# Performance work log

Hardware: AMD Instinct MI355X
Metric: run time of the kernel (lower is better)

The kernel has to match this reference:

```python
import jax, jax.numpy as jnp
import numpy as np


def setup_inputs() -> dict:
    key = jax.random.key(0)
    ks = jax.random.split(key, 6)
    b, c, h, w = 4, 64, 64, 64
    hid = 32
    x = jax.random.normal(ks[0], (b, c, h, w), dtype=jnp.float32)
    sc_in = 1.0 / np.sqrt(c)
    sc_hid = 1.0 / np.sqrt(hid)
    wq = jax.random.normal(ks[1], (hid, c), dtype=jnp.float32) * sc_in
    wk = jax.random.normal(ks[2], (hid, c), dtype=jnp.float32) * sc_in
    wv = jax.random.normal(ks[3], (hid, c), dtype=jnp.float32) * sc_in
    wp = jax.random.normal(ks[4], (c, hid), dtype=jnp.float32) * sc_hid
    bq = jnp.zeros((hid,), jnp.float32)
    bk = jnp.zeros((hid,), jnp.float32)
    bv = jnp.zeros((hid,), jnp.float32)
    bp = jnp.zeros((c,), jnp.float32)
    return {"x": x, "wq": wq, "bq": bq, "wk": wk, "bk": bk,
            "wv": wv, "bv": bv, "wp": wp, "bp": bp}


def reference(x, wq, bq, wk, bk, wv, bv, wp, bp):
    b, c, h, w = x.shape
    hid = wq.shape[0]
    # flatten spatial: [b, c, n]
    xf = x.reshape(b, c, h * w)
    # 1x1 convs == channel linear: q,k,v are [b, hid, n]
    q = jnp.einsum('oc,bcn->bon', wq, xf) + bq[None, :, None]
    k = jnp.einsum('oc,bcn->bon', wk, xf) + bk[None, :, None]
    v = jnp.einsum('oc,bcn->bon', wv, xf) + bv[None, :, None]
    # attention scores: query [b,n,hid] @ key [b,hid,m] -> [b,n,m] (NO scaling, as in source)
    scores = jnp.einsum('bhn,bhm->bnm', q, k)
    attn = jax.nn.softmax(scores, axis=-1)
    # z = attn @ value^T -> [b, n, hid] -> [b, hid, n]
    z = jnp.einsum('bnm,bhm->bhn', attn, v)
    # output projection (1x1 conv) + residual
    out = xf + jnp.einsum('ch,bhn->bcn', wp, z) + bp[None, :, None]
    return out.reshape(b, c, h, w)
```

## Files before the change

kernel.cpp:

```cpp
#include <hip/hip_runtime.h>
#include <hip/hip_bf16.h>
#include <math.h>

#define BB 4
#define CC 64
#define HID 32
#define NN 4096
#define LOG2E 1.44269504088896f

typedef short sh4 __attribute__((ext_vector_type(4)));
typedef short sh8 __attribute__((ext_vector_type(8)));
typedef float f4v __attribute__((ext_vector_type(4)));

#define MFMA32(A,B,C) __builtin_amdgcn_mfma_f32_16x16x32_bf16(A,B,C,0,0,0)

__device__ __forceinline__ short f2b(float f) {
    __hip_bfloat16 h = __float2bfloat16(f);
    union { __hip_bfloat16 hb; short s; } u; u.hb = h; return u.s;
}

__global__ __launch_bounds__(512) void qkv_kernel(
    const float* __restrict__ x,
    const float* __restrict__ wq, const float* __restrict__ bq,
    const float* __restrict__ wk, const float* __restrict__ bk,
    const float* __restrict__ wv, const float* __restrict__ bv,
    short* __restrict__ Qw, short* __restrict__ Kw, short* __restrict__ Vtp)
{
    __shared__ float xs[64][80];
    __shared__ float ws[96][80];
    __shared__ float bs[96];

    const int t  = threadIdx.x;
    const int b  = blockIdx.x >> 6;
    const int n0 = (blockIdx.x & 63) << 6;

    #pragma unroll
    for (int kl = 0; kl < 2; ++kl) {
        int idx = t + 512*kl;
        int c = idx >> 4, j4 = (idx & 15) << 2;
        *(f4v*)&xs[c][j4] = *(const f4v*)(x + ((size_t)(b*CC + c))*NN + n0 + j4);
    }
    #pragma unroll
    for (int kl = 0; kl < 3; ++kl) {
        int idx = t + 512*kl;
        int r = idx >> 4, c4 = (idx & 15) << 2;
        const float* src = (r < 32) ? (wq + r*CC + c4)
                         : (r < 64) ? (wk + (r-32)*CC + c4)
                                    : (wv + (r-64)*CC + c4);
        *(f4v*)&ws[r][c4] = *(const f4v*)src;
    }
    if (t < 96) bs[t] = (t < 32) ? bq[t] : (t < 64) ? bk[t-32] : bv[t-64];
    __syncthreads();

    const int hg = t & 31;
    const int j0 = (t >> 5) << 2;

    float aq[4], ak[4], av[4];
    #pragma unroll
    for (int jj = 0; jj < 4; ++jj) { aq[jj]=bs[hg]; ak[jj]=bs[32+hg]; av[jj]=bs[64+hg]; }

    #pragma unroll
    for (int cs = 0; cs < 16; ++cs) {
        f4v wqv = *(f4v*)&ws[hg][cs*4];
        f4v wkv = *(f4v*)&ws[32+hg][cs*4];
        f4v wvv = *(f4v*)&ws[64+hg][cs*4];
        #pragma unroll
        for (int cc = 0; cc < 4; ++cc) {
            f4v xv = *(f4v*)&xs[cs*4+cc][j0];
            #pragma unroll
            for (int jj = 0; jj < 4; ++jj) {
                aq[jj] += wqv[cc]*xv[jj];
                ak[jj] += wkv[cc]*xv[jj];
                av[jj] += wvv[cc]*xv[jj];
            }
        }
    }

    const size_t nbase = (size_t)b*NN + n0 + j0;
    #pragma unroll
    for (int jj = 0; jj < 4; ++jj) {
        Qw[(nbase + jj)*HID + hg] = f2b(aq[jj] * LOG2E);
        Kw[(nbase + jj)*HID + hg] = f2b(ak[jj]);
    }
    const int w0 = j0 & 31, g = (w0 >> 2) & 3, hi = w0 >> 4;
    sh4 vv;
    #pragma unroll
    for (int jj = 0; jj < 4; ++jj) vv[jj] = f2b(av[jj]);
    *(sh4*)(Vtp + ((size_t)b*HID + hg)*NN + n0 + (j0 & ~31) + 8*g + 4*hi) = vv;
}

__global__ __launch_bounds__(512, 2) void attn_kernel(
    const short* __restrict__ Qw, const short* __restrict__ Kw,
    const short* __restrict__ Vtp, const float* __restrict__ x,
    const float* __restrict__ wp, const float* __restrict__ bp,
    float* __restrict__ out)
{
    __shared__ float zr[4][32][65];
    __shared__ float lr4[4][64];

    const int t    = threadIdx.x;
    const int b    = blockIdx.x >> 6;
    const int q0   = (blockIdx.x & 63) << 6;
    const int lane = t & 63;
    const int kq   = t >> 6;
    const int g    = lane >> 4;
    const int qi   = lane & 15;

    const short* qbase = Qw + ((size_t)b*NN + q0 + qi)*HID + 8*g;
    sh8 qf[4];
    #pragma unroll
    for (int S = 0; S < 4; ++S) qf[S] = *(const sh8*)(qbase + S*16*HID);

    const short* kp = Kw  + ((size_t)b*NN  + kq*512 + qi)*HID + 8*g;
    const short* vp = Vtp + ((size_t)b*HID + qi)*NN + kq*512 + 8*g;

    const f4v zf = {0.f,0.f,0.f,0.f};
    f4v z0[4], z1[4], lz[4];
    #pragma unroll
    for (int S = 0; S < 4; ++S) { z0[S] = zf; z1[S] = zf; lz[S] = zf; }

    sh8 ones;
    #pragma unroll
    for (int j = 0; j < 8; ++j) ones[j] = (short)0x3F80;

    sh8 a0 = *(const sh8*)kp;
    sh8 a1 = *(const sh8*)(kp + 512);
    sh8 v0 = *(const sh8*)vp;
    sh8 v1 = *(const sh8*)(vp + 16*NN);

    for (int it = 0; it < 16; ++it) {
        const int nx = (it < 15) ? it + 1 : it;
        const short* kn = kp + nx*1024;
        const short* vn = vp + nx*32;
        sh8 na0 = *(const sh8*)kn;
        sh8 na1 = *(const sh8*)(kn + 512);
        sh8 nv0 = *(const sh8*)vn;
        sh8 nv1 = *(const sh8*)(vn + 16*NN);

        f4v s0[4], s1[4];
        #pragma unroll
        for (int S = 0; S < 4; ++S) {
            s0[S] = MFMA32(a0, qf[S], zf);
            s1[S] = MFMA32(a1, qf[S], zf);
        }

        sh8 p[4];
        #pragma unroll
        for (int S = 0; S < 4; ++S) {
            float e[8];
            #pragma unroll
            for (int r = 0; r < 4; ++r) {
                e[r]   = __builtin_amdgcn_exp2f(s0[S][r]);
                e[4+r] = __builtin_amdgcn_exp2f(s1[S][r]);
            }
            #pragma unroll
            for (int j = 0; j < 8; ++j) p[S][j] = f2b(e[j]);
        }

        #pragma unroll
        for (int S = 0; S < 4; ++S) {
            z0[S] = MFMA32(v0, p[S], z0[S]);
            z1[S] = MFMA32(v1, p[S], z1[S]);
            lz[S] = MFMA32(ones, p[S], lz[S]);
        }

        a0 = na0; a1 = na1; v0 = nv0; v1 = nv1;
    }

    if (kq >= 4) {
        #pragma unroll
        for (int S = 0; S < 4; ++S) {
            #pragma unroll
            for (int r = 0; r < 4; ++r) {
                zr[kq-4][4*g+r][S*16+qi]    = z0[S][r];
                zr[kq-4][16+4*g+r][S*16+qi] = z1[S][r];
            }
            if (g == 0) lr4[kq-4][S*16+qi] = lz[S][0];
        }
    }
    __syncthreads();
    if (kq < 4) {
        #pragma unroll
        for (int S = 0; S < 4; ++S) {
            #pragma unroll
            for (int r = 0; r < 4; ++r) {
                zr[kq][4*g+r][S*16+qi]    += z0[S][r];
                zr[kq][16+4*g+r][S*16+qi] += z1[S][r];
            }
            if (g == 0) lr4[kq][S*16+qi] += lz[S][0];
        }
    }
    __syncthreads();

    if (kq < 4) {
        const int q = kq*16 + qi;
        float lm = (lr4[0][q] + lr4[1][q]) + (lr4[2][q] + lr4[3][q]);
        f4v zm0 = zf, zm1 = zf;
        #pragma unroll
        for (int j = 0; j < 4; ++j) {
            #pragma unroll
            for (int r = 0; r < 4; ++r) {
                zm0[r] += zr[j][4*g+r][q];
                zm1[r] += zr[j][16+4*g+r][q];
            }
        }
        const float inv = 1.f / lm;
        sh8 pz;
        #pragma unroll
        for (int r = 0; r < 4; ++r) {
            pz[r]   = f2b(zm0[r]*inv);
            pz[4+r] = f2b(zm1[r]*inv);
        }
        const int qcol = q0 + q;
        #pragma unroll
        for (int ct = 0; ct < 4; ++ct) {
            const float* wrow = wp + (ct*16 + qi)*HID;
            f4v wa = *(const f4v*)(wrow + 4*g);
            f4v wb = *(const f4v*)(wrow + 16 + 4*g);
            sh8 af;
            #pragma unroll
            for (int i = 0; i < 4; ++i) { af[i] = f2b(wa[i]); af[4+i] = f2b(wb[i]); }
            f4v cacc;
            #pragma unroll
            for (int r = 0; r < 4; ++r) {
                int c = ct*16 + 4*g + r;
                cacc[r] = x[((size_t)(b*CC + c))*NN + qcol] + bp[c];
            }
            cacc = MFMA32(af, pz, cacc);
            #pragma unroll
            for (int r = 0; r < 4; ++r) {
                int c = ct*16 + 4*g + r;
                out[((size_t)(b*CC + c))*NN + qcol] = cacc[r];
            }
        }
    }
}

extern "C" void kernel_launch(void* const* d_in, const int* in_sizes, int n_in,
                              void* d_out, int out_size, void* d_ws, size_t ws_size,
                              hipStream_t stream) {
    const float* x  = (const float*)d_in[0];
    const float* wq = (const float*)d_in[1];
    const float* bq = (const float*)d_in[2];
    const float* wk = (const float*)d_in[3];
    const float* bk = (const float*)d_in[4];
    const float* wv = (const float*)d_in[5];
    const float* bv = (const float*)d_in[6];
    const float* wp = (const float*)d_in[7];
    const float* bp = (const float*)d_in[8];

    short* Qw  = (short*)d_ws;
    short* Kw  = Qw + (size_t)BB*NN*HID;
    short* Vtp = Kw + (size_t)BB*NN*HID;

    qkv_kernel<<<dim3(256), dim3(512), 0, stream>>>(x, wq, bq, wk, bk, wv, bv, Qw, Kw, Vtp);
    attn_kernel<<<dim3(256), dim3(512), 0, stream>>>(Qw, Kw, Vtp, x, wp, bp, (float*)d_out);
}
```

Baseline: 28.52 us.

## Double waves per block, split keys 16 ways, sum softmax denominators on VALU

Both kernels now launch 1024-thread blocks. The attention kernel splits the key range across 16 waves of 256 keys each instead of 8 waves of 512, which adds latency hiding on a grid that has only one block per CU. The row sum is now computed with VALU adds and cross-lane shuffles instead of an extra MFMA against a vector of ones, and the cross-wave reduction uses a transposed LDS layout read and written as float4. The costs are more LDS, tighter register limits from the new launch bounds (spill risk), and float4 LDS accesses on a 33-float row stride that are not 16-byte aligned.

Result: slower. 30.09 us, median of 3 (+5.5%).

```diff
diff --git a/kernel.cpp b/kernel.cpp
--- a/kernel.cpp
+++ b/kernel.cpp
@@ -8,8 +8,9 @@
 #define NN 4096
 #define LOG2E 1.44269504088896f
 
-typedef short sh4 __attribute__((ext_vector_type(4)));
+typedef short sh2 __attribute__((ext_vector_type(2)));
 typedef short sh8 __attribute__((ext_vector_type(8)));
+typedef float f2v __attribute__((ext_vector_type(2)));
 typedef float f4v __attribute__((ext_vector_type(4)));
 
 #define MFMA32(A,B,C) __builtin_amdgcn_mfma_f32_16x16x32_bf16(A,B,C,0,0,0)
@@ -19,45 +20,45 @@
     union { __hip_bfloat16 hb; short s; } u; u.hb = h; return u.s;
 }
 
-__global__ __launch_bounds__(512) void qkv_kernel(
+__global__ __launch_bounds__(1024) void qkv_kernel(
     const float* __restrict__ x,
     const float* __restrict__ wq, const float* __restrict__ bq,
     const float* __restrict__ wk, const float* __restrict__ bk,
     const float* __restrict__ wv, const float* __restrict__ bv,
     short* __restrict__ Qw, short* __restrict__ Kw, short* __restrict__ Vtp)
 {
-    __shared__ float xs[64][80];
-    __shared__ float ws[96][80];
+    __shared__ float xs[64][84];
+    __shared__ float ws[96][84];
     __shared__ float bs[96];
 
     const int t  = threadIdx.x;
     const int b  = blockIdx.x >> 6;
     const int n0 = (blockIdx.x & 63) << 6;
 
+    {
+        int c = t >> 4, j4 = (t & 15) << 2;
+        *(f4v*)&xs[c][j4] = *(const f4v*)(x + ((size_t)(b*CC + c))*NN + n0 + j4);
+    }
     #pragma unroll
     for (int kl = 0; kl < 2; ++kl) {
-        int idx = t + 512*kl;
-        int c = idx >> 4, j4 = (idx & 15) << 2;
-        *(f4v*)&xs[c][j4] = *(const f4v*)(x + ((size_t)(b*CC + c))*NN + n0 + j4);
-    }
-    #pragma unroll
-    for (int kl = 0; kl < 3; ++kl) {
-        int idx = t + 512*kl;
-        int r = idx >> 4, c4 = (idx & 15) << 2;
-        const float* src = (r < 32) ? (wq + r*CC + c4)
-                         : (r < 64) ? (wk + (r-32)*CC + c4)
-                                    : (wv + (r-64)*CC + c4);
-        *(f4v*)&ws[r][c4] = *(const f4v*)src;
+        int idx = t + 1024*kl;
+        if (idx < 1536) {
+            int r = idx >> 4, c4 = (idx & 15) << 2;
+            const float* src = (r < 32) ? (wq + r*CC + c4)
+                             : (r < 64) ? (wk + (r-32)*CC + c4)
+                                        : (wv + (r-64)*CC + c4);
+            *(f4v*)&ws[r][c4] = *(const f4v*)src;
+        }
     }
     if (t < 96) bs[t] = (t < 32) ? bq[t] : (t < 64) ? bk[t-32] : bv[t-64];
     __syncthreads();
 
     const int hg = t & 31;
-    const int j0 = (t >> 5) << 2;
-
-    float aq[4], ak[4], av[4];
-    #pragma unroll
-    for (int jj = 0; jj < 4; ++jj) { aq[jj]=bs[hg]; ak[jj]=bs[32+hg]; av[jj]=bs[64+hg]; }
+    const int j0 = (t >> 5) << 1;
+
+    float aq[2], ak[2], av[2];
+    #pragma unroll
+    for (int jj = 0; jj < 2; ++jj) { aq[jj]=bs[hg]; ak[jj]=bs[32+hg]; av[jj]=bs[64+hg]; }
 
     #pragma unroll
     for (int cs = 0; cs < 16; ++cs) {
@@ -66,9 +67,9 @@
         f4v wvv = *(f4v*)&ws[64+hg][cs*4];
         #pragma unroll
         for (int cc = 0; cc < 4; ++cc) {
-            f4v xv = *(f4v*)&xs[cs*4+cc][j0];
-            #pragma unroll
-            for (int jj = 0; jj < 4; ++jj) {
+            f2v xv = *(f2v*)&xs[cs*4+cc][j0];
+            #pragma unroll
+            for (int jj = 0; jj < 2; ++jj) {
                 aq[jj] += wqv[cc]*xv[jj];
                 ak[jj] += wkv[cc]*xv[jj];
                 av[jj] += wvv[cc]*xv[jj];
@@ -78,60 +79,56 @@
 
     const size_t nbase = (size_t)b*NN + n0 + j0;
     #pragma unroll
-    for (int jj = 0; jj < 4; ++jj) {
+    for (int jj = 0; jj < 2; ++jj) {
         Qw[(nbase + jj)*HID + hg] = f2b(aq[jj] * LOG2E);
         Kw[(nbase + jj)*HID + hg] = f2b(ak[jj]);
     }
-    const int w0 = j0 & 31, g = (w0 >> 2) & 3, hi = w0 >> 4;
-    sh4 vv;
-    #pragma unroll
-    for (int jj = 0; jj < 4; ++jj) vv[jj] = f2b(av[jj]);
-    *(sh4*)(Vtp + ((size_t)b*HID + hg)*NN + n0 + (j0 & ~31) + 8*g + 4*hi) = vv;
-}
-
-__global__ __launch_bounds__(512, 2) void attn_kernel(
+    const int w0  = j0 & 31;
+    const int pos = 8*((w0 >> 2) & 3) + (w0 & 3) + 4*(w0 >> 4);
+    sh2 vv; vv[0] = f2b(av[0]); vv[1] = f2b(av[1]);
+    *(sh2*)(Vtp + ((size_t)b*HID + hg)*NN + n0 + (j0 & ~31) + pos) = vv;
+}
+
+__global__ __launch_bounds__(1024, 4) void attn_kernel(
     const short* __restrict__ Qw, const short* __restrict__ Kw,
     const short* __restrict__ Vtp, const float* __restrict__ x,
     const float* __restrict__ wp, const float* __restrict__ bp,
     float* __restrict__ out)
 {
-    __shared__ float zr[4][32][65];
-    __shared__ float lr4[4][64];
+    __shared__ float zr[8][64][33];
+    __shared__ float lr[8][64];
 
     const int t    = threadIdx.x;
     const int b    = blockIdx.x >> 6;
     const int q0   = (blockIdx.x & 63) << 6;
     const int lane = t & 63;
-    const int kq   = t >> 6;
+    const int w    = t >> 6;
     const int g    = lane >> 4;
     const int qi   = lane & 15;
 
-    const short* qbase = Qw + ((size_t)b*NN + q0 + qi)*HID + 8*g;
     sh8 qf[4];
     #pragma unroll
-    for (int S = 0; S < 4; ++S) qf[S] = *(const sh8*)(qbase + S*16*HID);
-
-    const short* kp = Kw  + ((size_t)b*NN  + kq*512 + qi)*HID + 8*g;
-    const short* vp = Vtp + ((size_t)b*HID + qi)*NN + kq*512 + 8*g;
+    for (int S = 0; S < 4; ++S)
+        qf[S] = *(const sh8*)(Qw + ((size_t)b*NN + q0 + S*16 + qi)*HID + 8*g);
+
+    const short* kp = Kw  + ((size_t)b*NN  + w*256 + qi)*HID + 8*g;
+    const short* vp = Vtp + ((size_t)b*HID + qi)*NN + w*256 + 8*g;
 
     const f4v zf = {0.f,0.f,0.f,0.f};
-    f4v z0[4], z1[4], lz[4];
-    #pragma unroll
-    for (int S = 0; S < 4; ++S) { z0[S] = zf; z1[S] = zf; lz[S] = zf; }
-
-    sh8 ones;
-    #pragma unroll
-    for (int j = 0; j < 8; ++j) ones[j] = (short)0x3F80;
+    f4v z0[4], z1[4];
+    float lacc[4];
+    #pragma unroll
+    for (int S = 0; S < 4; ++S) { z0[S] = zf; z1[S] = zf; lacc[S] = 0.f; }
 
     sh8 a0 = *(const sh8*)kp;
     sh8 a1 = *(const sh8*)(kp + 512);
     sh8 v0 = *(const sh8*)vp;
     sh8 v1 = *(const sh8*)(vp + 16*NN);
 
-    for (int it = 0; it < 16; ++it) {
-        const int nx = (it < 15) ? it + 1 : it;
-        const short* kn = kp + nx*1024;
-        const short* vn = vp + nx*32;
+    for (int it = 0; it < 8; ++it) {
+        const int nx = (it < 7) ? it + 1 : it;
+        const short* kn = kp + (size_t)nx*1024;
+        const short* vn = vp + (size_t)nx*32;
         sh8 na0 = *(const sh8*)kn;
         sh8 na1 = *(const sh8*)(kn + 512);
         sh8 nv0 = *(const sh8*)vn;
@@ -153,6 +150,7 @@
                 e[r]   = __builtin_amdgcn_exp2f(s0[S][r]);
                 e[4+r] = __builtin_amdgcn_exp2f(s1[S][r]);
             }
+            lacc[S] += ((e[0]+e[1])+(e[2]+e[3])) + ((e[4]+e[5])+(e[6]+e[7]));
             #pragma unroll
             for (int j = 0; j < 8; ++j) p[S][j] = f2b(e[j]);
         }
@@ -161,48 +159,49 @@
         for (int S = 0; S < 4; ++S) {
             z0[S] = MFMA32(v0, p[S], z0[S]);
             z1[S] = MFMA32(v1, p[S], z1[S]);
-            lz[S] = MFMA32(ones, p[S], lz[S]);
         }
 
         a0 = na0; a1 = na1; v0 = nv0; v1 = nv1;
     }
 
-    if (kq >= 4) {
-        #pragma unroll
-        for (int S = 0; S < 4; ++S) {
-            #pragma unroll
-            for (int r = 0; r < 4; ++r) {
-                zr[kq-4][4*g+r][S*16+qi]    = z0[S][r];
-                zr[kq-4][16+4*g+r][S*16+qi] = z1[S][r];
-            }
-            if (g == 0) lr4[kq-4][S*16+qi] = lz[S][0];
+    #pragma unroll
+    for (int S = 0; S < 4; ++S) {
+        lacc[S] += __shfl_xor(lacc[S], 16, 64);
+        lacc[S] += __shfl_xor(lacc[S], 32, 64);
+    }
+
+    if (w >= 8) {
+        #pragma unroll
+        for (int S = 0; S < 4; ++S) {
+            *(f4v*)&zr[w-8][S*16 + qi][4*g]      = z0[S];
+            *(f4v*)&zr[w-8][S*16 + qi][16 + 4*g] = z1[S];
+            if (g == 0) lr[w-8][S*16 + qi] = lacc[S];
         }
     }
     __syncthreads();
-    if (kq < 4) {
-        #pragma unroll
-        for (int S = 0; S < 4; ++S) {
-            #pragma unroll
-            for (int r = 0; r < 4; ++r) {
-                zr[kq][4*g+r][S*16+qi]    += z0[S][r];
-                zr[kq][16+4*g+r][S*16+qi] += z1[S][r];
-            }
-            if (g == 0) lr4[kq][S*16+qi] += lz[S][0];
+    if (w < 8) {
+        #pragma unroll
+        for (int S = 0; S < 4; ++S) {
+            f4v ta = *(f4v*)&zr[w][S*16 + qi][4*g];
+            f4v tb = *(f4v*)&zr[w][S*16 + qi][16 + 4*g];
+            ta += z0[S]; tb += z1[S];
+            *(f4v*)&zr[w][S*16 + qi][4*g]      = ta;
+            *(f4v*)&zr[w][S*16 + qi][16 + 4*g] = tb;
+            if (g == 0) lr[w][S*16 + qi] += lacc[S];
         }
     }
     __syncthreads();
 
-    if (kq < 4) {
-        const int q = kq*16 + qi;
-        float lm = (lr4[0][q] + lr4[1][q]) + (lr4[2][q] + lr4[3][q]);
+    if (w < 4) {
+        const int q = w*16 + qi;
+        float lm = 0.f;
+        #pragma unroll
+        for (int s = 0; s < 8; ++s) lm += lr[s][q];
         f4v zm0 = zf, zm1 = zf;
         #pragma unroll
-        for (int j = 0; j < 4; ++j) {
-            #pragma unroll
-            for (int r = 0; r < 4; ++r) {
-                zm0[r] += zr[j][4*g+r][q];
-                zm1[r] += zr[j][16+4*g+r][q];
-            }
+        for (int s = 0; s < 8; ++s) {
+            zm0 += *(f4v*)&zr[s][q][4*g];
+            zm1 += *(f4v*)&zr[s][q][16 + 4*g];
         }
         const float inv = 1.f / lm;
         sh8 pz;
@@ -253,6 +252,6 @@
     short* Kw  = Qw + (size_t)BB*NN*HID;
     short* Vtp = Kw + (size_t)BB*NN*HID;
 
-    qkv_kernel<<<dim3(256), dim3(512), 0, stream>>>(x, wq, bq, wk, bk, wv, bv, Qw, Kw, Vtp);
-    attn_kernel<<<dim3(256), dim3(512), 0, stream>>>(Qw, Kw, Vtp, x, wp, bp, (float*)d_out);
-}
+    qkv_kernel<<<dim3(256), dim3(1024), 0, stream>>>(x, wq, bq, wk, bk, wv, bv, Qw, Kw, Vtp);
+    attn_kernel<<<dim3(256), dim3(1024), 0, stream>>>(Qw, Kw, Vtp, x, wp, bp, (float*)d_out);
+}
```
